# Kernel tuning notes

Hardware: AMD Instinct MI355X
Metric: run time of the kernel (lower is better)

Reference implementation:

```python
import jax, jax.numpy as jnp
import numpy as np

C = 32           # max_channels (in == out == 32, stride 1)
K = 3            # base kernel size
EXP_NITER = 5    # ConvExponential iterations -> effective kernel 11x11
POWER_IT = 3     # FantasticFour power iterations
B, H, W = 16, 256, 256


def _l2n(x):
    # L2Normalize over all dims (applied on store via right_inverse and again on read; idempotent)
    return x / (jnp.sqrt(jnp.sum(x * x)) + 1e-12)


def _skew(k):
    # K - flip(K^T, spatial)
    return k - jnp.flip(jnp.transpose(k, (1, 0, 2, 3)), axis=(2, 3))


def _fantastic_four(kernel, u1, u2, u3, u4):
    u1, u2, u3, u4 = map(_l2n, (u1, u2, u3, u4))
    for _ in range(POWER_IT):
        v1 = _l2n(jnp.sum(kernel * u1, axis=(1, 3), keepdims=True))
        u1 = _l2n(jnp.sum(kernel * v1, axis=(0, 2), keepdims=True))
        v2 = _l2n(jnp.sum(kernel * u2, axis=(1, 2), keepdims=True))
        u2 = _l2n(jnp.sum(kernel * v2, axis=(0, 3), keepdims=True))
        v3 = _l2n(jnp.sum(kernel * u3, axis=(1, 2, 3), keepdims=True))
        u3 = _l2n(jnp.sum(kernel * v3, axis=0, keepdims=True))
        v4 = _l2n(jnp.sum(kernel * u4, axis=(0, 2, 3), keepdims=True))
        u4 = _l2n(jnp.sum(kernel * v4, axis=1, keepdims=True))
    sg = jax.lax.stop_gradient  # sigmas use detached u/v, grad only via kernel
    s1 = jnp.sum(kernel * sg(u1) * sg(v1))
    s2 = jnp.sum(kernel * sg(u2) * sg(v2))
    s3 = jnp.sum(kernel * sg(u3) * sg(v3))
    s4 = jnp.sum(kernel * sg(u4) * sg(v4))
    sigma = jnp.minimum(jnp.minimum(s1, s2), jnp.minimum(s3, s4))
    return kernel / sigma


def _conv_exp(kernel):
    # kernel_global = I + K + K*K/2! + ... (kernel composition = full spatial convolution)
    p = (K - 1) // 2
    ident = jnp.pad(jnp.eye(C, dtype=kernel.dtype)[:, :, None, None],
                    ((0, 0), (0, 0), (p, p), (p, p)))
    kg = kernel + ident            # (C, C, K, K)
    ki = kernel
    rhs = jnp.flip(kernel, axis=(2, 3))  # flip -> lax correlation becomes full convolution
    for i in range(2, EXP_NITER + 1):
        # out[o,d,y,x] = sum_{c,p,q} ki[c,d,y-p,x-q] * kernel[o,c,p,q]
        inp = jnp.transpose(ki, (1, 0, 2, 3))  # (d, c, h, w) as NCHW
        out = jax.lax.conv_general_dilated(
            inp, rhs, window_strides=(1, 1),
            padding=[(K - 1, K - 1), (K - 1, K - 1)],
            dimension_numbers=('NCHW', 'OIHW', 'NCHW'))
        ki = jnp.transpose(out, (1, 0, 2, 3)) / float(i)
        kg = jnp.pad(kg, ((0, 0), (0, 0), (p, p), (p, p))) + ki
    return kg  # (C, C, 11, 11) for K=3, EXP_NITER=5


def reference(x, weight_raw, bias, u1, u2, u3, u4):
    w = _conv_exp(_fantastic_four(_skew(weight_raw), u1, u2, u3, u4))
    pad = w.shape[2] // 2  # 5
    z = jnp.pad(x, ((0, 0), (0, 0), (pad, pad), (pad, pad)), mode='wrap')  # circular
    z = jax.lax.conv_general_dilated(
        z, w, window_strides=(1, 1), padding='VALID',
        dimension_numbers=('NCHW', 'OIHW', 'NCHW'))
    return z + bias[None, :, None, None]


def setup_inputs() -> dict:
    key = jax.random.key(0)
    ks = jax.random.split(key, 7)
    return {
        'x': jax.random.normal(ks[0], (B, C, H, W), dtype=jnp.float32),
        'weight_raw': jax.random.normal(ks[1], (C, C, K, K), dtype=jnp.float32),
        'bias': jax.random.normal(ks[2], (C,), dtype=jnp.float32),
        'u1': jax.random.normal(ks[3], (1, C, 1, K), dtype=jnp.float32),
        'u2': jax.random.normal(ks[4], (1, C, K, 1), dtype=jnp.float32),
        'u3': jax.random.normal(ks[5], (1, C, K, K), dtype=jnp.float32),
        'u4': jax.random.normal(ks[6], (C, 1, K, K), dtype=jnp.float32),
    }
```

## Files before the change

kernel.cpp:

```cpp
#include <hip/hip_runtime.h>
#include <math.h>

typedef __bf16 bf16x8 __attribute__((ext_vector_type(8)));
typedef float f32x16 __attribute__((ext_vector_type(16)));
typedef unsigned int uint4v __attribute__((ext_vector_type(4)));

__device__ __forceinline__ unsigned short bf16_rne(float f) {
    unsigned u = __float_as_uint(f);
    unsigned r = u + 0x7fffu + ((u >> 16) & 1u);
    return (unsigned short)(r >> 16);
}
__device__ __forceinline__ float bf16_to_f(unsigned short h) {
    return __uint_as_float(((unsigned)h) << 16);
}

__device__ __forceinline__ float block_sum256(float v, float* red) {
    #pragma unroll
    for (int off = 32; off > 0; off >>= 1)
        v += __shfl_down(v, off, 64);
    const int tid = threadIdx.x;
    if ((tid & 63) == 0) red[tid >> 6] = v;
    __syncthreads();
    float tot = red[0] + red[1] + red[2] + red[3];
    __syncthreads();
    return tot;
}

__device__ __forceinline__ void l2n_lds(float* a, int n, float* red) {
    float s = 0.f;
    for (int i = threadIdx.x; i < n; i += 256) s += a[i] * a[i];
    const float tot = block_sum256(s, red);
    const float sc = 1.0f / (sqrtf(tot) + 1e-12f);
    for (int i = threadIdx.x; i < n; i += 256) a[i] *= sc;
    __syncthreads();
}

__global__ __launch_bounds__(256) void ff_kernel(
    const float* __restrict__ wr,
    const float* __restrict__ u1g, const float* __restrict__ u2g,
    const float* __restrict__ u3g, const float* __restrict__ u4g,
    float* __restrict__ kf_out)
{
    __shared__ float ks[9216];
    __shared__ float u1[96], v1[96], u2[96], v2[96];
    __shared__ float u3[288], u4[288], v3[32], v4[32];
    __shared__ float red[8];
    const int tid = threadIdx.x;

    for (int i = tid; i < 9216; i += 256) {
        int q  = i % 3;
        int p  = (i / 3) % 3;
        int ic = (i / 9) % 32;
        int oc = i / 288;
        ks[i] = wr[i] - wr[ic * 288 + oc * 9 + (2 - p) * 3 + (2 - q)];
    }
    if (tid < 96) { u1[tid] = u1g[tid]; u2[tid] = u2g[tid]; }
    for (int i = tid; i < 288; i += 256) { u3[i] = u3g[i]; u4[i] = u4g[i]; }
    __syncthreads();
    l2n_lds(u1, 96, red);
    l2n_lds(u2, 96, red);
    l2n_lds(u3, 288, red);
    l2n_lds(u4, 288, red);

    for (int it = 0; it < 3; ++it) {
        if (tid < 96) {
            int o = tid / 3, p = tid % 3;
            float s = 0.f;
            for (int i = 0; i < 32; ++i)
                for (int q = 0; q < 3; ++q)
                    s += ks[o * 288 + i * 9 + p * 3 + q] * u1[i * 3 + q];
            v1[tid] = s;
        }
        __syncthreads();
        l2n_lds(v1, 96, red);
        if (tid < 96) {
            int i = tid / 3, q = tid % 3;
            float s = 0.f;
            for (int o = 0; o < 32; ++o)
                for (int p = 0; p < 3; ++p)
                    s += ks[o * 288 + i * 9 + p * 3 + q] * v1[o * 3 + p];
            u1[tid] = s;
        }
        __syncthreads();
        l2n_lds(u1, 96, red);
        if (tid < 96) {
            int o = tid / 3, q = tid % 3;
            float s = 0.f;
            for (int i = 0; i < 32; ++i)
                for (int p = 0; p < 3; ++p)
                    s += ks[o * 288 + i * 9 + p * 3 + q] * u2[i * 3 + p];
            v2[tid] = s;
        }
        __syncthreads();
        l2n_lds(v2, 96, red);
        if (tid < 96) {
            int i = tid / 3, p = tid % 3;
            float s = 0.f;
            for (int o = 0; o < 32; ++o)
                for (int q = 0; q < 3; ++q)
                    s += ks[o * 288 + i * 9 + p * 3 + q] * v2[o * 3 + q];
            u2[tid] = s;
        }
        __syncthreads();
        l2n_lds(u2, 96, red);
        if (tid < 32) {
            float s = 0.f;
            for (int i = 0; i < 32; ++i)
                for (int pq = 0; pq < 9; ++pq)
                    s += ks[tid * 288 + i * 9 + pq] * u3[i * 9 + pq];
            v3[tid] = s;
        }
        __syncthreads();
        l2n_lds(v3, 32, red);
        for (int j = tid; j < 288; j += 256) {
            float s = 0.f;
            for (int o = 0; o < 32; ++o)
                s += ks[o * 288 + j] * v3[o];
            u3[j] = s;
        }
        __syncthreads();
        l2n_lds(u3, 288, red);
        if (tid < 32) {
            float s = 0.f;
            for (int o = 0; o < 32; ++o)
                for (int pq = 0; pq < 9; ++pq)
                    s += ks[o * 288 + tid * 9 + pq] * u4[o * 9 + pq];
            v4[tid] = s;
        }
        __syncthreads();
        l2n_lds(v4, 32, red);
        for (int j = tid; j < 288; j += 256) {
            int o = j / 9, pq = j - o * 9;
            float s = 0.f;
            for (int i = 0; i < 32; ++i)
                s += ks[o * 288 + i * 9 + pq] * v4[i];
            u4[j] = s;
        }
        __syncthreads();
        l2n_lds(u4, 288, red);
    }

    float p1 = 0.f, p2 = 0.f, p3 = 0.f, p4 = 0.f;
    for (int idx = tid; idx < 9216; idx += 256) {
        int q = idx % 3;
        int p = (idx / 3) % 3;
        int i = (idx / 9) % 32;
        int o = idx / 288;
        float k = ks[idx];
        p1 += k * u1[i * 3 + q] * v1[o * 3 + p];
        p2 += k * u2[i * 3 + p] * v2[o * 3 + q];
        p3 += k * u3[i * 9 + p * 3 + q] * v3[o];
        p4 += k * u4[o * 9 + p * 3 + q] * v4[i];
    }
    float s1 = block_sum256(p1, red);
    float s2 = block_sum256(p2, red);
    float s3 = block_sum256(p3, red);
    float s4 = block_sum256(p4, red);
    float sigma = fminf(fminf(s1, s2), fminf(s3, s4));
    for (int idx = tid; idx < 9216; idx += 256)
        kf_out[idx] = ks[idx] / sigma;
}

__global__ void initacc_kernel(const float* __restrict__ kf, float* __restrict__ wacc) {
    int idx = blockIdx.x * 256 + threadIdx.x;
    if (idx >= 123904) return;
    int o = idx / 3872;
    int rem = idx - o * 3872;
    int c = rem / 121;
    int yx = rem - c * 121;
    int y = yx / 11, x = yx - y * 11;
    float v = (o == c && y == 5 && x == 5) ? 1.0f : 0.0f;
    if (y >= 4 && y <= 6 && x >= 4 && x <= 6)
        v += kf[o * 288 + c * 9 + (y - 4) * 3 + (x - 4)];
    wacc[idx] = v;
}

__global__ void expstep_kernel(const float* __restrict__ kf, const float* __restrict__ ki,
                               float* __restrict__ ko, float* __restrict__ wacc,
                               int S, float scale)
{
    const int S2 = S + 2;
    const int off = (11 - S2) >> 1;
    const int o = blockIdx.x >> 5;
    const int d = blockIdx.x & 31;
    for (int yx = threadIdx.x; yx < S2 * S2; yx += blockDim.x) {
        int y = yx / S2, xx = yx - y * S2;
        float s = 0.f;
        for (int c = 0; c < 32; ++c) {
            const float* kfo = kf + o * 288 + c * 9;
            const float* kic = ki + (c * 32 + d) * S * S;
            #pragma unroll
            for (int p = 0; p < 3; ++p) {
                int yy = y - p;
                if (yy < 0 || yy >= S) continue;
                #pragma unroll
                for (int q = 0; q < 3; ++q) {
                    int xq = xx - q;
                    if (xq < 0 || xq >= S) continue;
                    s += kfo[p * 3 + q] * kic[yy * S + xq];
                }
            }
        }
        s *= scale;
        ko[(o * 32 + d) * S2 * S2 + yx] = s;
        wacc[(o * 32 + d) * 121 + (y + off) * 11 + (xx + off)] += s;
    }
}

__global__ void wprep_kernel(const float* __restrict__ wacc, uint4v* __restrict__ wbuf) {
    int idx = blockIdx.x * 256 + threadIdx.x;
    if (idx >= 30976) return;
    int lane  = idx & 63;
    int split = (idx >> 6) & 1;
    int ch    = (idx >> 7) & 1;
    int tap   = idx >> 8;
    int o     = lane & 31;
    int cbase = ch * 16 + ((lane >> 5) << 3);
    unsigned short v[8];
    #pragma unroll
    for (int j = 0; j < 8; ++j) {
        float w = wacc[o * 3872 + (cbase + j) * 121 + tap];
        unsigned short h = bf16_rne(w);
        v[j] = split ? bf16_rne(w - bf16_to_f(h)) : h;
    }
    uint4v u;
    u.x = (unsigned)v[0] | ((unsigned)v[1] << 16);
    u.y = (unsigned)v[2] | ((unsigned)v[3] << 16);
    u.z = (unsigned)v[4] | ((unsigned)v[5] << 16);
    u.w = (unsigned)v[6] | ((unsigned)v[7] << 16);
    wbuf[idx] = u;
}

__global__ __launch_bounds__(256, 2) void conv_mfma_kernel(
    const float* __restrict__ x, const uint4v* __restrict__ wbuf,
    const float* __restrict__ bias, float* __restrict__ out)
{
    __shared__ unsigned short shi[2 * 1092 * 8];
    __shared__ unsigned short slo[2 * 1092 * 8];
    __shared__ float biasS[32];

    const int b    = blockIdx.z;
    const int Y0   = blockIdx.y << 4;
    const int X0   = blockIdx.x << 5;
    const int tid  = threadIdx.x;
    const int lane = tid & 63;
    const int ywave = (tid >> 6) << 2;
    const int myoff = (lane & 31) + (lane >> 5) * 1092;

    if (tid < 32) biasS[tid] = bias[tid];

    f32x16 acc[4];
    #pragma unroll
    for (int s = 0; s < 4; ++s)
        #pragma unroll
        for (int r = 0; r < 16; ++r) acc[s][r] = 0.f;

    const uint4v* ph = (const uint4v*)shi;
    const uint4v* pl = (const uint4v*)slo;

    for (int chlf = 0; chlf < 2; ++chlf) {
        __syncthreads();
        const float* xb = x + (((size_t)(b * 32 + chlf * 16)) << 16);
        for (int pix = tid; pix < 1092; pix += 256) {
            int r = pix / 42, s = pix - r * 42;
            int gy = (Y0 + r - 5) & 255;
            int gx = (X0 + s - 5) & 255;
            const float* xp = xb + (gy << 8) + gx;
            unsigned short hv[16], lv[16];
            #pragma unroll
            for (int cc = 0; cc < 16; ++cc) {
                float v = xp[(size_t)cc << 16];
                unsigned short h = bf16_rne(v);
                hv[cc] = h;
                lv[cc] = bf16_rne(v - bf16_to_f(h));
            }
            uint4v u;
            u.x = (unsigned)hv[0] | ((unsigned)hv[1] << 16);
            u.y = (unsigned)hv[2] | ((unsigned)hv[3] << 16);
            u.z = (unsigned)hv[4] | ((unsigned)hv[5] << 16);
            u.w = (unsigned)hv[6] | ((unsigned)hv[7] << 16);
            *(uint4v*)&shi[pix * 8] = u;
            u.x = (unsigned)hv[8]  | ((unsigned)hv[9]  << 16);
            u.y = (unsigned)hv[10] | ((unsigned)hv[11] << 16);
            u.z = (unsigned)hv[12] | ((unsigned)hv[13] << 16);
            u.w = (unsigned)hv[14] | ((unsigned)hv[15] << 16);
            *(uint4v*)&shi[(1092 + pix) * 8] = u;
            u.x = (unsigned)lv[0] | ((unsigned)lv[1] << 16);
            u.y = (unsigned)lv[2] | ((unsigned)lv[3] << 16);
            u.z = (unsigned)lv[4] | ((unsigned)lv[5] << 16);
            u.w = (unsigned)lv[6] | ((unsigned)lv[7] << 16);
            *(uint4v*)&slo[pix * 8] = u;
            u.x = (unsigned)lv[8]  | ((unsigned)lv[9]  << 16);
            u.y = (unsigned)lv[10] | ((unsigned)lv[11] << 16);
            u.z = (unsigned)lv[12] | ((unsigned)lv[13] << 16);
            u.w = (unsigned)lv[14] | ((unsigned)lv[15] << 16);
            *(uint4v*)&slo[(1092 + pix) * 8] = u;
        }
        __syncthreads();

        const int wb0 = chlf * 128 + lane;
        #pragma unroll 1
        for (int q = 0; q < 11; ++q) {
            uint4v ah[8], al[8];
            ah[0] = wbuf[wb0 + q * 256];
            al[0] = wbuf[wb0 + q * 256 + 64];
            ah[1] = wbuf[wb0 + (11 + q) * 256];
            al[1] = wbuf[wb0 + (11 + q) * 256 + 64];
            ah[2] = wbuf[wb0 + (22 + q) * 256];
            al[2] = wbuf[wb0 + (22 + q) * 256 + 64];
            bf16x8 Bh = __builtin_bit_cast(bf16x8, ph[ywave * 42 + q + myoff]);
            bf16x8 Bl = __builtin_bit_cast(bf16x8, pl[ywave * 42 + q + myoff]);
            #pragma unroll
            for (int r = 0; r < 14; ++r) {
                const bf16x8 cBh = Bh, cBl = Bl;
                if (r < 13) {
                    const int basen = (ywave + r + 1) * 42 + q + myoff;
                    Bh = __builtin_bit_cast(bf16x8, ph[basen]);
                    Bl = __builtin_bit_cast(bf16x8, pl[basen]);
                }
                if (r + 3 <= 10) {
                    ah[(r + 3) & 7] = wbuf[wb0 + ((r + 3) * 11 + q) * 256];
                    al[(r + 3) & 7] = wbuf[wb0 + ((r + 3) * 11 + q) * 256 + 64];
                }
                const int plo = (r - 3 > 0) ? r - 3 : 0;
                const int phi = (r < 10) ? r : 10;
                #pragma unroll
                for (int p = plo; p <= phi; ++p)
                    acc[r - p] = __builtin_amdgcn_mfma_f32_32x32x16_bf16(
                        __builtin_bit_cast(bf16x8, ah[p & 7]), cBh, acc[r - p], 0, 0, 0);
                #pragma unroll
                for (int p = plo; p <= phi; ++p)
                    acc[r - p] = __builtin_amdgcn_mfma_f32_32x32x16_bf16(
                        __builtin_bit_cast(bf16x8, al[p & 7]), cBh, acc[r - p], 0, 0, 0);
                #pragma unroll
                for (int p = plo; p <= phi; ++p)
                    acc[r - p] = __builtin_amdgcn_mfma_f32_32x32x16_bf16(
                        __builtin_bit_cast(bf16x8, ah[p & 7]), cBl, acc[r - p], 0, 0, 0);
            }
        }
    }

    const int colx = X0 + (lane & 31);
    const int half = lane >> 5;
    #pragma unroll
    for (int s = 0; s < 4; ++s) {
        int y = Y0 + ywave + s;
        #pragma unroll
        for (int r = 0; r < 16; ++r) {
            int o = (r & 3) + ((r >> 2) << 3) + (half << 2);
            out[(((size_t)(b * 32 + o)) << 16) + (y << 8) + colx] = acc[s][r] + biasS[o];
        }
    }
}

extern "C" void kernel_launch(void* const* d_in, const int* in_sizes, int n_in,
                              void* d_out, int out_size, void* d_ws, size_t ws_size,
                              hipStream_t stream) {
    const float* x    = (const float*)d_in[0];
    const float* wraw = (const float*)d_in[1];
    const float* bias = (const float*)d_in[2];
    const float* u1   = (const float*)d_in[3];
    const float* u2   = (const float*)d_in[4];
    const float* u3   = (const float*)d_in[5];
    const float* u4   = (const float*)d_in[6];
    float* out = (float*)d_out;

    float* ws   = (float*)d_ws;
    float* kf   = ws;
    float* bufA = kf + 9216;
    float* bufB = bufA + 123904;
    float* wacc = bufB + 123904;
    uint4v* wbuf = (uint4v*)(wacc + 123904);

    ff_kernel<<<1, 256, 0, stream>>>(wraw, u1, u2, u3, u4, kf);
    initacc_kernel<<<484, 256, 0, stream>>>(kf, wacc);
    expstep_kernel<<<1024, 128, 0, stream>>>(kf, kf,   bufA, wacc, 3, 0.5f);
    expstep_kernel<<<1024, 128, 0, stream>>>(kf, bufA, bufB, wacc, 5, 1.0f / 3.0f);
    expstep_kernel<<<1024, 128, 0, stream>>>(kf, bufB, bufA, wacc, 7, 0.25f);
    expstep_kernel<<<1024, 128, 0, stream>>>(kf, bufA, bufB, wacc, 9, 0.2f);
    wprep_kernel<<<121, 256, 0, stream>>>(wacc, wbuf);

    conv_mfma_kernel<<<dim3(8, 16, 16), 256, 0, stream>>>(x, wbuf, bias, out);
}
```

Before: 903.0 us.

## Overlap next channel-half staging with MFMA phases via split hi/lo buffers

Result: slower. 931.7 us (+3.2%).

```diff
diff --git a/kernel.cpp b/kernel.cpp
--- a/kernel.cpp
+++ b/kernel.cpp
@@ -231,12 +231,94 @@
     wbuf[idx] = u;
 }
 
+__device__ __forceinline__ void pack2(unsigned short* dst, const unsigned short* v) {
+    uint4v u;
+    u.x = (unsigned)v[0] | ((unsigned)v[1] << 16);
+    u.y = (unsigned)v[2] | ((unsigned)v[3] << 16);
+    u.z = (unsigned)v[4] | ((unsigned)v[5] << 16);
+    u.w = (unsigned)v[6] | ((unsigned)v[7] << 16);
+    *(uint4v*)dst = u;
+}
+
+template<bool TWOPASS, bool DOSTAGE, bool STHI>
+__device__ __forceinline__ void mfma_phase(
+    f32x16 (&acc)[4],
+    const uint4v* __restrict__ wbuf,
+    const uint4v* __restrict__ pb,
+    unsigned short* __restrict__ dst,
+    int schlf,
+    int chlf,
+    const float* __restrict__ x,
+    int b, int Y0, int X0, int tid, int lane, int ywave, int myoff)
+{
+    const int wb0 = chlf * 128 + lane;
+    #pragma unroll 1
+    for (int q = 0; q < 11; ++q) {
+        if (DOSTAGE) {
+            if (!(q & 1) && (q >> 1) < 5) {
+                int pix = tid + ((q >> 1) << 8);
+                if (pix < 1092) {
+                    int rr = pix / 42, ss = pix - rr * 42;
+                    int gy = (Y0 + rr - 5) & 255;
+                    int gx = (X0 + ss - 5) & 255;
+                    const float* xp = x + (((size_t)(b * 32 + schlf * 16)) << 16)
+                                        + (gy << 8) + gx;
+                    unsigned short wv[16];
+                    #pragma unroll
+                    for (int cc = 0; cc < 16; ++cc) {
+                        float v = xp[(size_t)cc << 16];
+                        unsigned short h = bf16_rne(v);
+                        wv[cc] = STHI ? h : bf16_rne(v - bf16_to_f(h));
+                    }
+                    pack2(&dst[pix * 8], wv);
+                    pack2(&dst[(1092 + pix) * 8], wv + 8);
+                }
+            }
+        }
+        uint4v ah[8], al[8];
+        ah[0] = wbuf[wb0 + q * 256];
+        ah[1] = wbuf[wb0 + (11 + q) * 256];
+        ah[2] = wbuf[wb0 + (22 + q) * 256];
+        if (TWOPASS) {
+            al[0] = wbuf[wb0 + q * 256 + 64];
+            al[1] = wbuf[wb0 + (11 + q) * 256 + 64];
+            al[2] = wbuf[wb0 + (22 + q) * 256 + 64];
+        }
+        bf16x8 B = __builtin_bit_cast(bf16x8, pb[ywave * 42 + q + myoff]);
+        #pragma unroll
+        for (int r = 0; r < 14; ++r) {
+            const bf16x8 cB = B;
+            if (r < 13)
+                B = __builtin_bit_cast(bf16x8, pb[(ywave + r + 1) * 42 + q + myoff]);
+            if (r + 3 <= 10) {
+                ah[(r + 3) & 7] = wbuf[wb0 + ((r + 3) * 11 + q) * 256];
+                if (TWOPASS)
+                    al[(r + 3) & 7] = wbuf[wb0 + ((r + 3) * 11 + q) * 256 + 64];
+            }
+            const int plo = (r - 3 > 0) ? r - 3 : 0;
+            const int phi = (r < 10) ? r : 10;
+            __builtin_amdgcn_s_setprio(1);
+            #pragma unroll
+            for (int p = plo; p <= phi; ++p)
+                acc[r - p] = __builtin_amdgcn_mfma_f32_32x32x16_bf16(
+                    __builtin_bit_cast(bf16x8, ah[p & 7]), cB, acc[r - p], 0, 0, 0);
+            if (TWOPASS) {
+                #pragma unroll
+                for (int p = plo; p <= phi; ++p)
+                    acc[r - p] = __builtin_amdgcn_mfma_f32_32x32x16_bf16(
+                        __builtin_bit_cast(bf16x8, al[p & 7]), cB, acc[r - p], 0, 0, 0);
+            }
+            __builtin_amdgcn_s_setprio(0);
+        }
+    }
+}
+
 __global__ __launch_bounds__(256, 2) void conv_mfma_kernel(
     const float* __restrict__ x, const uint4v* __restrict__ wbuf,
     const float* __restrict__ bias, float* __restrict__ out)
 {
-    __shared__ unsigned short shi[2 * 1092 * 8];
-    __shared__ unsigned short slo[2 * 1092 * 8];
+    __shared__ unsigned short bufA[2 * 1092 * 8];
+    __shared__ unsigned short bufB[2 * 1092 * 8];
     __shared__ float biasS[32];
 
     const int b    = blockIdx.z;
@@ -255,12 +337,8 @@
         #pragma unroll
         for (int r = 0; r < 16; ++r) acc[s][r] = 0.f;
 
-    const uint4v* ph = (const uint4v*)shi;
-    const uint4v* pl = (const uint4v*)slo;
-
-    for (int chlf = 0; chlf < 2; ++chlf) {
-        __syncthreads();
-        const float* xb = x + (((size_t)(b * 32 + chlf * 16)) << 16);
+    {
+        const float* xb = x + (((size_t)(b * 32)) << 16);
         for (int pix = tid; pix < 1092; pix += 256) {
             int r = pix / 42, s = pix - r * 42;
             int gy = (Y0 + r - 5) & 255;
@@ -274,71 +352,28 @@
                 hv[cc] = h;
                 lv[cc] = bf16_rne(v - bf16_to_f(h));
             }
-            uint4v u;
-            u.x = (unsigned)hv[0] | ((unsigned)hv[1] << 16);
-            u.y = (unsigned)hv[2] | ((unsigned)hv[3] << 16);
-            u.z = (unsigned)hv[4] | ((unsigned)hv[5] << 16);
-            u.w = (unsigned)hv[6] | ((unsigned)hv[7] << 16);
-            *(uint4v*)&shi[pix * 8] = u;
-            u.x = (unsigned)hv[8]  | ((unsigned)hv[9]  << 16);
-            u.y = (unsigned)hv[10] | ((unsigned)hv[11] << 16);
-            u.z = (unsigned)hv[12] | ((unsigned)hv[13] << 16);
-            u.w = (unsigned)hv[14] | ((unsigned)hv[15] << 16);
-            *(uint4v*)&shi[(1092 + pix) * 8] = u;
-            u.x = (unsigned)lv[0] | ((unsigned)lv[1] << 16);
-            u.y = (unsigned)lv[2] | ((unsigned)lv[3] << 16);
-            u.z = (unsigned)lv[4] | ((unsigned)lv[5] << 16);
-            u.w = (unsigned)lv[6] | ((unsigned)lv[7] << 16);
-            *(uint4v*)&slo[pix * 8] = u;
-            u.x = (unsigned)lv[8]  | ((unsigned)lv[9]  << 16);
-            u.y = (unsigned)lv[10] | ((unsigned)lv[11] << 16);
-            u.z = (unsigned)lv[12] | ((unsigned)lv[13] << 16);
-            u.w = (unsigned)lv[14] | ((unsigned)lv[15] << 16);
-            *(uint4v*)&slo[(1092 + pix) * 8] = u;
-        }
-        __syncthreads();
-
-        const int wb0 = chlf * 128 + lane;
-        #pragma unroll 1
-        for (int q = 0; q < 11; ++q) {
-            uint4v ah[8], al[8];
-            ah[0] = wbuf[wb0 + q * 256];
-            al[0] = wbuf[wb0 + q * 256 + 64];
-            ah[1] = wbuf[wb0 + (11 + q) * 256];
-            al[1] = wbuf[wb0 + (11 + q) * 256 + 64];
-            ah[2] = wbuf[wb0 + (22 + q) * 256];
-            al[2] = wbuf[wb0 + (22 + q) * 256 + 64];
-            bf16x8 Bh = __builtin_bit_cast(bf16x8, ph[ywave * 42 + q + myoff]);
-            bf16x8 Bl = __builtin_bit_cast(bf16x8, pl[ywave * 42 + q + myoff]);
-            #pragma unroll
-            for (int r = 0; r < 14; ++r) {
-                const bf16x8 cBh = Bh, cBl = Bl;
-                if (r < 13) {
-                    const int basen = (ywave + r + 1) * 42 + q + myoff;
-                    Bh = __builtin_bit_cast(bf16x8, ph[basen]);
-                    Bl = __builtin_bit_cast(bf16x8, pl[basen]);
-                }
-                if (r + 3 <= 10) {
-                    ah[(r + 3) & 7] = wbuf[wb0 + ((r + 3) * 11 + q) * 256];
-                    al[(r + 3) & 7] = wbuf[wb0 + ((r + 3) * 11 + q) * 256 + 64];
-                }
-                const int plo = (r - 3 > 0) ? r - 3 : 0;
-                const int phi = (r < 10) ? r : 10;
-                #pragma unroll
-                for (int p = plo; p <= phi; ++p)
-                    acc[r - p] = __builtin_amdgcn_mfma_f32_32x32x16_bf16(
-                        __builtin_bit_cast(bf16x8, ah[p & 7]), cBh, acc[r - p], 0, 0, 0);
-                #pragma unroll
-                for (int p = plo; p <= phi; ++p)
-                    acc[r - p] = __builtin_amdgcn_mfma_f32_32x32x16_bf16(
-                        __builtin_bit_cast(bf16x8, al[p & 7]), cBh, acc[r - p], 0, 0, 0);
-                #pragma unroll
-                for (int p = plo; p <= phi; ++p)
-                    acc[r - p] = __builtin_amdgcn_mfma_f32_32x32x16_bf16(
-                        __builtin_bit_cast(bf16x8, ah[p & 7]), cBl, acc[r - p], 0, 0, 0);
-            }
-        }
-    }
+            pack2(&bufA[pix * 8], hv);
+            pack2(&bufA[(1092 + pix) * 8], hv + 8);
+            pack2(&bufB[pix * 8], lv);
+            pack2(&bufB[(1092 + pix) * 8], lv + 8);
+        }
+    }
+    __syncthreads();
+
+    mfma_phase<true, false, false>(acc, wbuf, (const uint4v*)bufA, nullptr, 0, 0,
+                                   x, b, Y0, X0, tid, lane, ywave, myoff);
+    __syncthreads();
+
+    mfma_phase<false, true, true>(acc, wbuf, (const uint4v*)bufB, bufA, 1, 0,
+                                  x, b, Y0, X0, tid, lane, ywave, myoff);
+    __syncthreads();
+
+    mfma_phase<true, true, false>(acc, wbuf, (const uint4v*)bufA, bufB, 1, 1,
+                                  x, b, Y0, X0, tid, lane, ywave, myoff);
+    __syncthreads();
+
+    mfma_phase<false, false, false>(acc, wbuf, (const uint4v*)bufB, nullptr, 1, 1,
+                                    x, b, Y0, X0, tid, lane, ywave, myoff);
 
     const int colx = X0 + (lane & 31);
     const int half = lane >> 5;
```

## Fuse FantasticFour and conv-exponential steps into one per-column weight kernel

Applied to the files above, without the earlier changes.

After: 881.5 us. -2.4%, faster.

```diff
diff --git a/kernel.cpp b/kernel.cpp
--- a/kernel.cpp
+++ b/kernel.cpp
@@ -35,17 +35,64 @@
     __syncthreads();
 }
 
-__global__ __launch_bounds__(256) void ff_kernel(
+template<int SIN, bool LAST>
+__device__ __forceinline__ void exp_step(
+    const float* __restrict__ ks, const float* __restrict__ kin,
+    float* __restrict__ kout, float* __restrict__ waccS,
+    float scale, int tid)
+{
+    constexpr int S2  = SIN + 2;
+    constexpr int OFF = (11 - S2) / 2;
+    constexpr int NCH = (S2 + 3) / 4;
+    constexpr int TOT = 32 * S2 * NCH;
+    for (int ch = tid; ch < TOT; ch += 256) {
+        int o   = ch / (S2 * NCH);
+        int rem = ch - o * (S2 * NCH);
+        int y   = rem / NCH;
+        int x0  = (rem - y * NCH) * 4;
+        float a0 = 0.f, a1 = 0.f, a2 = 0.f, a3 = 0.f;
+        for (int c = 0; c < 32; ++c) {
+            const float* kfo = ks + o * 288 + c * 9;
+            #pragma unroll
+            for (int p = 0; p < 3; ++p) {
+                const float* row = kin + c * 182 + (y + 2 - p) * 14 + x0;
+                float w0 = row[0], w1 = row[1], w2 = row[2];
+                float w3 = row[3], w4 = row[4], w5 = row[5];
+                float k0 = kfo[p * 3], k1 = kfo[p * 3 + 1], k2 = kfo[p * 3 + 2];
+                a0 += k0 * w2; a0 += k1 * w1; a0 += k2 * w0;
+                a1 += k0 * w3; a1 += k1 * w2; a1 += k2 * w1;
+                a2 += k0 * w4; a2 += k1 * w3; a2 += k2 * w2;
+                a3 += k0 * w5; a3 += k1 * w4; a3 += k2 * w3;
+            }
+        }
+        a0 *= scale; a1 *= scale; a2 *= scale; a3 *= scale;
+        float av[4] = {a0, a1, a2, a3};
+        #pragma unroll
+        for (int dx = 0; dx < 4; ++dx) {
+            int xx = x0 + dx;
+            if (xx < S2) {
+                if (!LAST) kout[o * 182 + (y + 2) * 14 + (xx + 2)] = av[dx];
+                waccS[o * 121 + (y + OFF) * 11 + (xx + OFF)] += av[dx];
+            }
+        }
+    }
+}
+
+__global__ __launch_bounds__(256) void weight_kernel(
     const float* __restrict__ wr,
     const float* __restrict__ u1g, const float* __restrict__ u2g,
     const float* __restrict__ u3g, const float* __restrict__ u4g,
-    float* __restrict__ kf_out)
+    float* __restrict__ wacc)
 {
     __shared__ float ks[9216];
+    __shared__ float kiA[32 * 182];
+    __shared__ float kiB[32 * 182];
+    __shared__ float waccS[32 * 121];
     __shared__ float u1[96], v1[96], u2[96], v2[96];
     __shared__ float u3[288], u4[288], v3[32], v4[32];
     __shared__ float red[8];
     const int tid = threadIdx.x;
+    const int d   = blockIdx.x;
 
     for (int i = tid; i < 9216; i += 256) {
         int q  = i % 3;
@@ -158,52 +205,44 @@
     float s4 = block_sum256(p4, red);
     float sigma = fminf(fminf(s1, s2), fminf(s3, s4));
     for (int idx = tid; idx < 9216; idx += 256)
-        kf_out[idx] = ks[idx] / sigma;
-}
-
-__global__ void initacc_kernel(const float* __restrict__ kf, float* __restrict__ wacc) {
-    int idx = blockIdx.x * 256 + threadIdx.x;
-    if (idx >= 123904) return;
-    int o = idx / 3872;
-    int rem = idx - o * 3872;
-    int c = rem / 121;
-    int yx = rem - c * 121;
-    int y = yx / 11, x = yx - y * 11;
-    float v = (o == c && y == 5 && x == 5) ? 1.0f : 0.0f;
-    if (y >= 4 && y <= 6 && x >= 4 && x <= 6)
-        v += kf[o * 288 + c * 9 + (y - 4) * 3 + (x - 4)];
-    wacc[idx] = v;
-}
-
-__global__ void expstep_kernel(const float* __restrict__ kf, const float* __restrict__ ki,
-                               float* __restrict__ ko, float* __restrict__ wacc,
-                               int S, float scale)
-{
-    const int S2 = S + 2;
-    const int off = (11 - S2) >> 1;
-    const int o = blockIdx.x >> 5;
-    const int d = blockIdx.x & 31;
-    for (int yx = threadIdx.x; yx < S2 * S2; yx += blockDim.x) {
-        int y = yx / S2, xx = yx - y * S2;
-        float s = 0.f;
-        for (int c = 0; c < 32; ++c) {
-            const float* kfo = kf + o * 288 + c * 9;
-            const float* kic = ki + (c * 32 + d) * S * S;
-            #pragma unroll
-            for (int p = 0; p < 3; ++p) {
-                int yy = y - p;
-                if (yy < 0 || yy >= S) continue;
-                #pragma unroll
-                for (int q = 0; q < 3; ++q) {
-                    int xq = xx - q;
-                    if (xq < 0 || xq >= S) continue;
-                    s += kfo[p * 3 + q] * kic[yy * S + xq];
-                }
-            }
-        }
-        s *= scale;
-        ko[(o * 32 + d) * S2 * S2 + yx] = s;
-        wacc[(o * 32 + d) * 121 + (y + off) * 11 + (xx + off)] += s;
+        ks[idx] = ks[idx] / sigma;
+    __syncthreads();
+
+    for (int i = tid; i < 32 * 182; i += 256) kiA[i] = 0.f;
+    for (int i = tid; i < 3872; i += 256) {
+        int o = i / 121, j = i - o * 121;
+        int y = j / 11, xx = j - y * 11;
+        float v = (o == d && y == 5 && xx == 5) ? 1.0f : 0.0f;
+        if (y >= 4 && y <= 6 && xx >= 4 && xx <= 6)
+            v += ks[o * 288 + d * 9 + (y - 4) * 3 + (xx - 4)];
+        waccS[i] = v;
+    }
+    __syncthreads();
+    for (int i = tid; i < 288; i += 256) {
+        int c = i / 9, t = i - c * 9;
+        int yy = t / 3, xx = t - yy * 3;
+        kiA[c * 182 + (yy + 2) * 14 + (xx + 2)] = ks[c * 288 + d * 9 + t];
+    }
+    __syncthreads();
+
+    for (int i = tid; i < 32 * 182; i += 256) kiB[i] = 0.f;
+    __syncthreads();
+    exp_step<3, false>(ks, kiA, kiB, waccS, 0.5f, tid);
+    __syncthreads();
+    for (int i = tid; i < 32 * 182; i += 256) kiA[i] = 0.f;
+    __syncthreads();
+    exp_step<5, false>(ks, kiB, kiA, waccS, 1.0f / 3.0f, tid);
+    __syncthreads();
+    for (int i = tid; i < 32 * 182; i += 256) kiB[i] = 0.f;
+    __syncthreads();
+    exp_step<7, false>(ks, kiA, kiB, waccS, 0.25f, tid);
+    __syncthreads();
+    exp_step<9, true>(ks, kiB, kiA, waccS, 0.2f, tid);
+    __syncthreads();
+
+    for (int i = tid; i < 3872; i += 256) {
+        int o = i / 121, j = i - o * 121;
+        wacc[(o * 32 + d) * 121 + j] = waccS[i];
     }
 }
 
@@ -366,19 +405,10 @@
     float* out = (float*)d_out;
 
     float* ws   = (float*)d_ws;
-    float* kf   = ws;
-    float* bufA = kf + 9216;
-    float* bufB = bufA + 123904;
-    float* wacc = bufB + 123904;
+    float* wacc = ws;
     uint4v* wbuf = (uint4v*)(wacc + 123904);
 
-    ff_kernel<<<1, 256, 0, stream>>>(wraw, u1, u2, u3, u4, kf);
-    initacc_kernel<<<484, 256, 0, stream>>>(kf, wacc);
-    expstep_kernel<<<1024, 128, 0, stream>>>(kf, kf,   bufA, wacc, 3, 0.5f);
-    expstep_kernel<<<1024, 128, 0, stream>>>(kf, bufA, bufB, wacc, 5, 1.0f / 3.0f);
-    expstep_kernel<<<1024, 128, 0, stream>>>(kf, bufB, bufA, wacc, 7, 0.25f);
-    expstep_kernel<<<1024, 128, 0, stream>>>(kf, bufA, bufB, wacc, 9, 0.2f);
+    weight_kernel<<<32, 256, 0, stream>>>(wraw, u1, u2, u3, u4, wacc);
     wprep_kernel<<<121, 256, 0, stream>>>(wacc, wbuf);
-
     conv_mfma_kernel<<<dim3(8, 16, 16), 256, 0, stream>>>(x, wbuf, bias, out);
 }
```
